# Kernel tuning notes

Hardware: AMD Instinct MI355X
Metric: run time of the kernel (lower is better)

The kernel has to match this reference:

```python
import jax, jax.numpy as jnp
import numpy as np

N = 50000      # nodes
E = 400000     # edges (avg degree 8)
N_IN = 256     # n_in_chan
N_HID = 256    # n_hid_chan


def gcn_conv(x, src, dst, W, b, n):
    """PyG GCNConv: D^{-1/2}(A+I)D^{-1/2} X W^T + b (add_self_loops=True, unit weights)."""
    h = x @ W.T                                           # [n, out]
    # degree over A + I: each node has a self loop (the initial ones) plus in-edges
    deg = jnp.ones((n,), h.dtype).at[dst].add(1.0)        # [n]
    dinv = jax.lax.rsqrt(deg)                             # deg >= 1 always
    norm = dinv[src] * dinv[dst]                          # [E]
    agg = jnp.zeros_like(h).at[dst].add(h[src] * norm[:, None])
    agg = agg + h * (dinv * dinv)[:, None]                # self-loop term, norm = dinv_i^2
    return agg + b


def setup_inputs() -> dict:
    key = jax.random.key(0)
    k1, k2, k3, k4 = jax.random.split(key, 4)
    x = jax.random.normal(k1, (N, N_IN + N_HID), dtype=jnp.float32)
    edge_index = jax.random.randint(k2, (2, E), 0, N, dtype=jnp.int64)
    s1 = 1.0 / np.sqrt(N_IN + N_HID)
    s2 = 1.0 / np.sqrt(N_HID)
    W1 = jax.random.normal(k3, (N_HID, N_IN + N_HID), dtype=jnp.float32) * s1
    W2 = jax.random.normal(k4, (N_HID, N_HID), dtype=jnp.float32) * s2
    b1 = jnp.zeros((N_HID,), jnp.float32)
    b2 = jnp.zeros((N_HID,), jnp.float32)
    return {"x": x, "edge_index": edge_index, "W1": W1, "b1": b1, "W2": W2, "b2": b2}


def reference(x, edge_index, W1, b1, W2, b2):
    src, dst = edge_index[0], edge_index[1]
    h = jax.nn.relu(gcn_conv(x, src, dst, W1, b1, N))
    return gcn_conv(h, src, dst, W2, b2, N)
```

## Files before the change

kernel.cpp:

```cpp
#include <hip/hip_runtime.h>

#define NN 50000
#define CH 256

typedef unsigned short u16;
typedef unsigned int   u32;

using short8 = __attribute__((ext_vector_type(8))) short;
using f32x4  = __attribute__((ext_vector_type(4))) float;

static __device__ __forceinline__ float4 ld4(const float* p){ return *(const float4*)p; }

static __device__ __forceinline__ u16 f2b(float f){
  u32 u = __float_as_uint(f);
  u = (u + 0x7fffu + ((u >> 16) & 1u)) >> 16;
  return (u16)u;
}
static __device__ __forceinline__ float b2f(u16 b){
  return __uint_as_float(((u32)b) << 16);
}


__global__ void hist_kernel(const int* __restrict__ dst, int* __restrict__ cnt, int E){
  int e = blockIdx.x*256 + threadIdx.x;
  if (e < E) atomicAdd(&cnt[dst[e]], 1);
}

__global__ void dinv_kernel(const int* __restrict__ cnt, float* __restrict__ dinv, int n){
  int i = blockIdx.x*256 + threadIdx.x;
  if (i < n) dinv[i] = rsqrtf(1.0f + (float)cnt[i]);
}

__global__ void scan_partial_kernel(const int* __restrict__ cnt, int* __restrict__ bsum, int n){
  __shared__ int sd[256];
  int t = threadIdx.x;
  int base = blockIdx.x*1024 + t*4;
  int s = 0;
  #pragma unroll
  for (int j=0;j<4;j++){ int idx = base+j; if (idx<n) s += cnt[idx]; }
  sd[t] = s; __syncthreads();
  for (int off=128; off>0; off>>=1){ if (t<off) sd[t]+=sd[t+off]; __syncthreads(); }
  if (t==0) bsum[blockIdx.x] = sd[0];
}

__global__ void scan_bsums_kernel(int* __restrict__ bsum, int nb){
  int t = threadIdx.x;
  int v = (t < nb) ? bsum[t] : 0;
  int orig = v;
  #pragma unroll
  for (int off=1; off<64; off<<=1){
    int u = __shfl_up(v, off, 64);
    if (t >= off) v += u;
  }
  if (t < nb) bsum[t] = v - orig;
}

__global__ void scan_final_kernel(const int* __restrict__ cnt, const int* __restrict__ bsum,
                                  int* __restrict__ offs, int* __restrict__ cursor, int n, int total){
  __shared__ int sd[256];
  int t = threadIdx.x;
  int base = blockIdx.x*1024 + t*4;
  int v[4]; int s=0;
  #pragma unroll
  for (int j=0;j<4;j++){ int idx=base+j; v[j] = (idx<n)?cnt[idx]:0; s += v[j]; }
  sd[t]=s; __syncthreads();
  for (int off=1; off<256; off<<=1){
    int x = (t>=off)? sd[t-off] : 0;
    __syncthreads();
    sd[t] += x;
    __syncthreads();
  }
  int run = bsum[blockIdx.x] + sd[t] - s;
  #pragma unroll
  for (int j=0;j<4;j++){
    int idx=base+j;
    if (idx<n){ offs[idx]=run; cursor[idx]=run; }
    run += v[j];
  }
  if (blockIdx.x==0 && t==0) offs[n] = total;
}

__global__ void scatter_kernel(const int* __restrict__ src, const int* __restrict__ dst,
                               const float* __restrict__ dinv, int* __restrict__ cursor,
                               int* __restrict__ esrc, float* __restrict__ enorm, int E){
  int e = blockIdx.x*256 + threadIdx.x;
  if (e < E){
    int d = dst[e], s = src[e];
    int pos = atomicAdd(&cursor[d], 1);
    esrc[pos] = s;
    enorm[pos] = dinv[s]*dinv[d];
  }
}


__global__ __launch_bounds__(256) void cvt_kernel(const float* __restrict__ in,
                                                  u16* __restrict__ out, int n4){
  int i = blockIdx.x*256 + threadIdx.x;
  if (i >= n4) return;
  float4 v = ld4(in + (size_t)i*4);
  ushort4 o;
  o.x = f2b(v.x); o.y = f2b(v.y); o.z = f2b(v.z); o.w = f2b(v.w);
  *(ushort4*)(out + (size_t)i*4) = o;
}


static __device__ __forceinline__ void gload_lds16(const u16* g, u16* l){
  __builtin_amdgcn_global_load_lds((const __attribute__((address_space(1))) void*)g,
                                   (__attribute__((address_space(3))) void*)l, 16, 0, 0);
}

__global__ __launch_bounds__(256) void gemm_mfma_kernel(const u16* __restrict__ A,
                                                        const u16* __restrict__ B,
                                                        u16* __restrict__ C,
                                                        int M, int K){
  __shared__ u16 As[128*32];
  __shared__ u16 Bs[128*32];
  int tid = threadIdx.x;
  int wave = tid >> 6, lane = tid & 63;
  int bm = blockIdx.x, bn = blockIdx.y;

  int sr = tid >> 2;
  int sc = (tid & 3) * 8;
  int ar0 = bm*128 + sr;       if (ar0 > M-1) ar0 = M-1;
  int ar1 = bm*128 + 64 + sr;  if (ar1 > M-1) ar1 = M-1;
  const u16* ga0 = A + (size_t)ar0*K + sc;
  const u16* ga1 = A + (size_t)ar1*K + sc;
  const u16* gb0 = B + (size_t)(bn*128 + sr)*K + sc;
  const u16* gb1 = B + (size_t)(bn*128 + 64 + sr)*K + sc;
  u16* la0 = As + (size_t)(wave*64)*8;
  u16* la1 = As + (size_t)(256 + wave*64)*8;
  u16* lb0 = Bs + (size_t)(wave*64)*8;
  u16* lb1 = Bs + (size_t)(256 + wave*64)*8;

  int wm = wave & 1, wn = wave >> 1;
  int lm = lane & 15;
  int lk = (lane >> 4) * 8;

  f32x4 acc[4][4] = {};

  for (int k0 = 0; k0 < K; k0 += 32){
    gload_lds16(ga0 + k0, la0);
    gload_lds16(ga1 + k0, la1);
    gload_lds16(gb0 + k0, lb0);
    gload_lds16(gb1 + k0, lb1);
    __syncthreads();
    short8 af[4], bfr[4];
    #pragma unroll
    for (int i=0;i<4;i++)
      af[i] = *(const short8*)&As[(size_t)(wm*64 + i*16 + lm)*32 + lk];
    #pragma unroll
    for (int j=0;j<4;j++)
      bfr[j] = *(const short8*)&Bs[(size_t)(wn*64 + j*16 + lm)*32 + lk];
    #pragma unroll
    for (int i=0;i<4;i++)
      #pragma unroll
      for (int j=0;j<4;j++)
        acc[i][j] = __builtin_amdgcn_mfma_f32_16x16x32_bf16(af[i], bfr[j], acc[i][j], 0, 0, 0);
    __syncthreads();
  }

  int rb = (lane >> 4) * 4;
  #pragma unroll
  for (int i=0;i<4;i++){
    #pragma unroll
    for (int r=0;r<4;r++){
      int row = bm*128 + wm*64 + i*16 + rb + r;
      if (row < M){
        #pragma unroll
        for (int j=0;j<4;j++){
          int col = bn*128 + wn*64 + j*16 + lm;
          C[(size_t)row*CH + col] = f2b(acc[i][j][r]);
        }
      }
    }
  }
}


template<bool RELU, bool OUTBF>
__global__ __launch_bounds__(256) void aggregate_kernel(const u16* __restrict__ h,
                                                        const float* __restrict__ bias,
                                                        const float* __restrict__ dinv,
                                                        const int* __restrict__ offs,
                                                        const int* __restrict__ esrc,
                                                        const float* __restrict__ enorm,
                                                        void* __restrict__ outv, int n){
  int wave = threadIdx.x >> 6;
  int lane = threadIdx.x & 63;
  int i = blockIdx.x*4 + wave;
  if (i >= n) return;
  int c = lane*4;
  float di = dinv[i];
  float w = di*di;
  float4 b4 = ld4(bias + c);
  ushort4 hv = *(const ushort4*)(h + (size_t)i*CH + c);
  float a0 = b2f(hv.x)*w + b4.x;
  float a1 = b2f(hv.y)*w + b4.y;
  float a2 = b2f(hv.z)*w + b4.z;
  float a3 = b2f(hv.w)*w + b4.w;
  int e0 = offs[i], e1 = offs[i+1];
  int e = e0;
  for (; e + 1 < e1; e += 2){
    int s0 = esrc[e], s1 = esrc[e+1];
    float n0 = enorm[e], n1 = enorm[e+1];
    ushort4 h0 = *(const ushort4*)(h + (size_t)s0*CH + c);
    ushort4 h1 = *(const ushort4*)(h + (size_t)s1*CH + c);
    a0 += b2f(h0.x)*n0; a1 += b2f(h0.y)*n0; a2 += b2f(h0.z)*n0; a3 += b2f(h0.w)*n0;
    a0 += b2f(h1.x)*n1; a1 += b2f(h1.y)*n1; a2 += b2f(h1.z)*n1; a3 += b2f(h1.w)*n1;
  }
  if (e < e1){
    int s0 = esrc[e];
    float n0 = enorm[e];
    ushort4 h0 = *(const ushort4*)(h + (size_t)s0*CH + c);
    a0 += b2f(h0.x)*n0; a1 += b2f(h0.y)*n0; a2 += b2f(h0.z)*n0; a3 += b2f(h0.w)*n0;
  }
  if (RELU){
    a0 = fmaxf(a0,0.f); a1 = fmaxf(a1,0.f); a2 = fmaxf(a2,0.f); a3 = fmaxf(a3,0.f);
  }
  if (OUTBF){
    ushort4 o; o.x=f2b(a0); o.y=f2b(a1); o.z=f2b(a2); o.w=f2b(a3);
    *(ushort4*)((u16*)outv + (size_t)i*CH + c) = o;
  } else {
    *(float4*)((float*)outv + (size_t)i*CH + c) = make_float4(a0,a1,a2,a3);
  }
}


extern "C" void kernel_launch(void* const* d_in, const int* in_sizes, int n_in,
                              void* d_out, int out_size, void* d_ws, size_t ws_size,
                              hipStream_t stream){
  const float* x  = (const float*)d_in[0];
  const int*   ei = (const int*)d_in[1];
  const float* W1 = (const float*)d_in[2];
  const float* b1 = (const float*)d_in[3];
  const float* W2 = (const float*)d_in[4];
  const float* b2 = (const float*)d_in[5];
  float* out = (float*)d_out;

  const int n = NN;
  const int E = in_sizes[1] / 2;
  const int* src = ei;
  const int* dst = ei + E;
  const int KIN = in_sizes[0] / n;

  char* ws = (char*)d_ws;
  size_t off = 0;
  auto alloc = [&](size_t bytes)->char* {
    char* p = ws + off;
    off += (bytes + 255) & ~(size_t)255;
    return p;
  };
  u16*   Xbf    = (u16*)  alloc((size_t)n*KIN*sizeof(u16));
  u16*   W1bf   = (u16*)  alloc((size_t)CH*KIN*sizeof(u16));
  u16*   W2bf   = (u16*)  alloc((size_t)CH*CH*sizeof(u16));
  float* dinv   = (float*)alloc((size_t)n*sizeof(float));
  int*   cnt    = (int*)  alloc((size_t)n*sizeof(int));
  int*   offs   = (int*)  alloc((size_t)(n+1)*sizeof(int));
  int*   cursor = (int*)  alloc((size_t)n*sizeof(int));
  int*   bsum   = (int*)  alloc(256*sizeof(int));
  int*   esrc   = (int*)  alloc((size_t)E*sizeof(int));
  float* enorm  = (float*)alloc((size_t)E*sizeof(float));
  (void)ws_size;

  u16* g1out = (u16*)d_out;
  u16* h1bf  = Xbf;
  u16* g2out = Xbf + (size_t)n*CH;

  hipMemsetAsync(cnt, 0, (size_t)n*sizeof(int), stream);
  hist_kernel<<<(E+255)/256, 256, 0, stream>>>(dst, cnt, E);
  dinv_kernel<<<(n+255)/256, 256, 0, stream>>>(cnt, dinv, n);
  int nb = (n + 1023) / 1024;
  scan_partial_kernel<<<nb, 256, 0, stream>>>(cnt, bsum, n);
  scan_bsums_kernel<<<1, 64, 0, stream>>>(bsum, nb);
  scan_final_kernel<<<nb, 256, 0, stream>>>(cnt, bsum, offs, cursor, n, E);
  scatter_kernel<<<(E+255)/256, 256, 0, stream>>>(src, dst, dinv, cursor, esrc, enorm, E);

  cvt_kernel<<<(n*KIN/4+255)/256, 256, 0, stream>>>(x, Xbf, n*KIN/4);
  cvt_kernel<<<(CH*KIN/4+255)/256, 256, 0, stream>>>(W1, W1bf, CH*KIN/4);
  cvt_kernel<<<(CH*CH/4+255)/256, 256, 0, stream>>>(W2, W2bf, CH*CH/4);

  dim3 gg((n+127)/128, CH/128);
  gemm_mfma_kernel<<<gg, 256, 0, stream>>>(Xbf, W1bf, g1out, n, KIN);
  aggregate_kernel<true, true><<<(n+3)/4, 256, 0, stream>>>(g1out, b1, dinv, offs, esrc, enorm, h1bf, n);

  gemm_mfma_kernel<<<gg, 256, 0, stream>>>(h1bf, W2bf, g2out, n, CH);
  aggregate_kernel<false, false><<<(n+3)/4, 256, 0, stream>>>(g2out, b2, dinv, offs, esrc, enorm, out, n);
}
```

Before: 356.9 us.

## Fuse graph setup and conversions into one cooperative kernel; widen aggregation loads

Replaces the histogram, dinv, three scan kernels, the CSR scatter and the three bf16 conversion kernels with a single cooperative-launch kernel that uses grid-wide syncs between phases. The X conversion overlaps with the block-sum scan. The aggregation kernel now gives each half-wave alternate edges, uses 8-wide bf16 loads and combines the halves with a cross-lane shuffle. The goal is to cut launch overhead and raise memory-level parallelism in the gather, at the cost of grid-sync latency and a fixed 512-block setup grid.

```diff
diff --git a/kernel.cpp b/kernel.cpp
--- a/kernel.cpp
+++ b/kernel.cpp
@@ -1,12 +1,17 @@
 #include <hip/hip_runtime.h>
+#include <hip/hip_cooperative_groups.h>
+
+namespace cg = cooperative_groups;
 
 #define NN 50000
 #define CH 256
+#define SETUP_BLOCKS 512
 
 typedef unsigned short u16;
 typedef unsigned int   u32;
 
 using short8 = __attribute__((ext_vector_type(8))) short;
+using u16x8  = __attribute__((ext_vector_type(8))) unsigned short;
 using f32x4  = __attribute__((ext_vector_type(4))) float;
 
 static __device__ __forceinline__ float4 ld4(const float* p){ return *(const float4*)p; }
@@ -21,86 +26,104 @@
 }
 
 
-__global__ void hist_kernel(const int* __restrict__ dst, int* __restrict__ cnt, int E){
-  int e = blockIdx.x*256 + threadIdx.x;
-  if (e < E) atomicAdd(&cnt[dst[e]], 1);
-}
-
-__global__ void dinv_kernel(const int* __restrict__ cnt, float* __restrict__ dinv, int n){
-  int i = blockIdx.x*256 + threadIdx.x;
-  if (i < n) dinv[i] = rsqrtf(1.0f + (float)cnt[i]);
-}
-
-__global__ void scan_partial_kernel(const int* __restrict__ cnt, int* __restrict__ bsum, int n){
+__global__ __launch_bounds__(256) void setup_kernel(const float* __restrict__ x,
+                                                    const float* __restrict__ W1,
+                                                    const float* __restrict__ W2,
+                                                    const int* __restrict__ src,
+                                                    const int* __restrict__ dst,
+                                                    u16* __restrict__ Xbf,
+                                                    u16* __restrict__ W1bf,
+                                                    u16* __restrict__ W2bf,
+                                                    float* __restrict__ dinv,
+                                                    int* __restrict__ cnt,
+                                                    int* __restrict__ offs,
+                                                    int* __restrict__ cursor,
+                                                    int* __restrict__ bsum,
+                                                    int* __restrict__ esrc,
+                                                    float* __restrict__ enorm,
+                                                    int n, int E, int KIN){
+  cg::grid_group grid = cg::this_grid();
   __shared__ int sd[256];
-  int t = threadIdx.x;
-  int base = blockIdx.x*1024 + t*4;
-  int s = 0;
-  #pragma unroll
-  for (int j=0;j<4;j++){ int idx = base+j; if (idx<n) s += cnt[idx]; }
-  sd[t] = s; __syncthreads();
-  for (int off=128; off>0; off>>=1){ if (t<off) sd[t]+=sd[t+off]; __syncthreads(); }
-  if (t==0) bsum[blockIdx.x] = sd[0];
-}
-
-__global__ void scan_bsums_kernel(int* __restrict__ bsum, int nb){
-  int t = threadIdx.x;
-  int v = (t < nb) ? bsum[t] : 0;
-  int orig = v;
-  #pragma unroll
-  for (int off=1; off<64; off<<=1){
-    int u = __shfl_up(v, off, 64);
-    if (t >= off) v += u;
-  }
-  if (t < nb) bsum[t] = v - orig;
-}
-
-__global__ void scan_final_kernel(const int* __restrict__ cnt, const int* __restrict__ bsum,
-                                  int* __restrict__ offs, int* __restrict__ cursor, int n, int total){
-  __shared__ int sd[256];
-  int t = threadIdx.x;
-  int base = blockIdx.x*1024 + t*4;
-  int v[4]; int s=0;
-  #pragma unroll
-  for (int j=0;j<4;j++){ int idx=base+j; v[j] = (idx<n)?cnt[idx]:0; s += v[j]; }
-  sd[t]=s; __syncthreads();
-  for (int off=1; off<256; off<<=1){
-    int x = (t>=off)? sd[t-off] : 0;
-    __syncthreads();
-    sd[t] += x;
-    __syncthreads();
-  }
-  int run = bsum[blockIdx.x] + sd[t] - s;
-  #pragma unroll
-  for (int j=0;j<4;j++){
-    int idx=base+j;
-    if (idx<n){ offs[idx]=run; cursor[idx]=run; }
-    run += v[j];
-  }
-  if (blockIdx.x==0 && t==0) offs[n] = total;
-}
-
-__global__ void scatter_kernel(const int* __restrict__ src, const int* __restrict__ dst,
-                               const float* __restrict__ dinv, int* __restrict__ cursor,
-                               int* __restrict__ esrc, float* __restrict__ enorm, int E){
-  int e = blockIdx.x*256 + threadIdx.x;
-  if (e < E){
+  const int t = threadIdx.x;
+  const int b = blockIdx.x;
+  const int T = gridDim.x * 256;
+  const int g = b*256 + t;
+  const int nb2 = (n + 255) / 256;
+
+  for (int i = g; i < n; i += T) cnt[i] = 0;
+  int w1n = CH*KIN/4;
+  for (int i = g; i < w1n; i += T){
+    float4 v = ld4(W1 + (size_t)i*4);
+    ushort4 o; o.x=f2b(v.x); o.y=f2b(v.y); o.z=f2b(v.z); o.w=f2b(v.w);
+    *(ushort4*)(W1bf + (size_t)i*4) = o;
+  }
+  int w2n = CH*CH/4;
+  for (int i = g; i < w2n; i += T){
+    float4 v = ld4(W2 + (size_t)i*4);
+    ushort4 o; o.x=f2b(v.x); o.y=f2b(v.y); o.z=f2b(v.z); o.w=f2b(v.w);
+    *(ushort4*)(W2bf + (size_t)i*4) = o;
+  }
+  grid.sync();
+
+  for (int e = g; e < E; e += T) atomicAdd(&cnt[dst[e]], 1);
+  grid.sync();
+
+  if (b < nb2){
+    int i = b*256 + t;
+    int v = (i < n) ? cnt[i] : 0;
+    if (i < n) dinv[i] = rsqrtf(1.0f + (float)v);
+    sd[t] = v; __syncthreads();
+    #pragma unroll
+    for (int off=1; off<256; off<<=1){
+      int u = (t>=off) ? sd[t-off] : 0;
+      __syncthreads();
+      sd[t] += u;
+      __syncthreads();
+    }
+    if (i < n) offs[i] = sd[t];
+    if (t == 255) bsum[b] = sd[255];
+  }
+  grid.sync();
+
+  if (b == 0){
+    int v = (t < nb2) ? bsum[t] : 0;
+    sd[t] = v; __syncthreads();
+    #pragma unroll
+    for (int off=1; off<256; off<<=1){
+      int u = (t>=off) ? sd[t-off] : 0;
+      __syncthreads();
+      sd[t] += u;
+      __syncthreads();
+    }
+    if (t < nb2) bsum[t] = sd[t] - v;
+  } else {
+    int xn = n*(KIN/4);
+    int T3 = (gridDim.x-1)*256;
+    for (int i = (b-1)*256 + t; i < xn; i += T3){
+      float4 v = ld4(x + (size_t)i*4);
+      ushort4 o; o.x=f2b(v.x); o.y=f2b(v.y); o.z=f2b(v.z); o.w=f2b(v.w);
+      *(ushort4*)(Xbf + (size_t)i*4) = o;
+    }
+  }
+  grid.sync();
+
+  if (b < nb2){
+    int i = b*256 + t;
+    if (i < n){
+      int ex = bsum[b] + offs[i] - cnt[i];
+      offs[i] = ex;
+      cursor[i] = ex;
+    }
+  }
+  if (g == 0) offs[n] = E;
+  grid.sync();
+
+  for (int e = g; e < E; e += T){
     int d = dst[e], s = src[e];
     int pos = atomicAdd(&cursor[d], 1);
     esrc[pos] = s;
     enorm[pos] = dinv[s]*dinv[d];
   }
-}
-
-
-__global__ __launch_bounds__(256) void cvt_kernel(const float* __restrict__ in,
-                                                  u16* __restrict__ out, int n4){
-  int i = blockIdx.x*256 + threadIdx.x;
-  if (i >= n4) return;
-  float4 v = ld4(in + (size_t)i*4);
-  ushort4 o;
-  o.x = f2b(v.x); o.y = f2b(v.y); o.z = f2b(v.z); o.w = f2b(v.w);
-  *(ushort4*)(out + (size_t)i*4) = o;
 }
 
 
@@ -189,39 +212,62 @@
   int lane = threadIdx.x & 63;
   int i = blockIdx.x*4 + wave;
   if (i >= n) return;
-  int c = lane*4;
-  float di = dinv[i];
-  float w = di*di;
-  float4 b4 = ld4(bias + c);
-  ushort4 hv = *(const ushort4*)(h + (size_t)i*CH + c);
-  float a0 = b2f(hv.x)*w + b4.x;
-  float a1 = b2f(hv.y)*w + b4.y;
-  float a2 = b2f(hv.z)*w + b4.z;
-  float a3 = b2f(hv.w)*w + b4.w;
+  int half = lane >> 5;
+  int c = (lane & 31) * 8;
+
+  float acc[8];
+  u16x8 hv = *(const u16x8*)(h + (size_t)i*CH + c);
+  if (half == 0){
+    float di = dinv[i];
+    float w = di*di;
+    float4 b0 = ld4(bias + c), b1 = ld4(bias + c + 4);
+    acc[0]=b2f(hv[0])*w+b0.x; acc[1]=b2f(hv[1])*w+b0.y;
+    acc[2]=b2f(hv[2])*w+b0.z; acc[3]=b2f(hv[3])*w+b0.w;
+    acc[4]=b2f(hv[4])*w+b1.x; acc[5]=b2f(hv[5])*w+b1.y;
+    acc[6]=b2f(hv[6])*w+b1.z; acc[7]=b2f(hv[7])*w+b1.w;
+  } else {
+    #pragma unroll
+    for (int k=0;k<8;k++) acc[k] = 0.f;
+  }
+
   int e0 = offs[i], e1 = offs[i+1];
-  int e = e0;
-  for (; e + 1 < e1; e += 2){
-    int s0 = esrc[e], s1 = esrc[e+1];
-    float n0 = enorm[e], n1 = enorm[e+1];
-    ushort4 h0 = *(const ushort4*)(h + (size_t)s0*CH + c);
-    ushort4 h1 = *(const ushort4*)(h + (size_t)s1*CH + c);
-    a0 += b2f(h0.x)*n0; a1 += b2f(h0.y)*n0; a2 += b2f(h0.z)*n0; a3 += b2f(h0.w)*n0;
-    a0 += b2f(h1.x)*n1; a1 += b2f(h1.y)*n1; a2 += b2f(h1.z)*n1; a3 += b2f(h1.w)*n1;
+  int e = e0 + half;
+  for (; e + 2 < e1; e += 4){
+    int sA = esrc[e],   sB = esrc[e+2];
+    float nA = enorm[e], nB = enorm[e+2];
+    u16x8 hA = *(const u16x8*)(h + (size_t)sA*CH + c);
+    u16x8 hB = *(const u16x8*)(h + (size_t)sB*CH + c);
+    #pragma unroll
+    for (int k=0;k<8;k++) acc[k] += b2f(hA[k])*nA;
+    #pragma unroll
+    for (int k=0;k<8;k++) acc[k] += b2f(hB[k])*nB;
   }
   if (e < e1){
-    int s0 = esrc[e];
-    float n0 = enorm[e];
-    ushort4 h0 = *(const ushort4*)(h + (size_t)s0*CH + c);
-    a0 += b2f(h0.x)*n0; a1 += b2f(h0.y)*n0; a2 += b2f(h0.z)*n0; a3 += b2f(h0.w)*n0;
-  }
-  if (RELU){
-    a0 = fmaxf(a0,0.f); a1 = fmaxf(a1,0.f); a2 = fmaxf(a2,0.f); a3 = fmaxf(a3,0.f);
-  }
-  if (OUTBF){
-    ushort4 o; o.x=f2b(a0); o.y=f2b(a1); o.z=f2b(a2); o.w=f2b(a3);
-    *(ushort4*)((u16*)outv + (size_t)i*CH + c) = o;
-  } else {
-    *(float4*)((float*)outv + (size_t)i*CH + c) = make_float4(a0,a1,a2,a3);
+    int sA = esrc[e];
+    float nA = enorm[e];
+    u16x8 hA = *(const u16x8*)(h + (size_t)sA*CH + c);
+    #pragma unroll
+    for (int k=0;k<8;k++) acc[k] += b2f(hA[k])*nA;
+  }
+
+  #pragma unroll
+  for (int k=0;k<8;k++) acc[k] += __shfl_xor(acc[k], 32, 64);
+
+  if (half == 0){
+    if (RELU){
+      #pragma unroll
+      for (int k=0;k<8;k++) acc[k] = fmaxf(acc[k], 0.f);
+    }
+    if (OUTBF){
+      u16x8 o;
+      #pragma unroll
+      for (int k=0;k<8;k++) o[k] = f2b(acc[k]);
+      *(u16x8*)((u16*)outv + (size_t)i*CH + c) = o;
+    } else {
+      float* op = (float*)outv + (size_t)i*CH + c;
+      *(float4*)op       = make_float4(acc[0],acc[1],acc[2],acc[3]);
+      *(float4*)(op + 4) = make_float4(acc[4],acc[5],acc[6],acc[7]);
+    }
   }
 }
 
@@ -266,18 +312,16 @@
   u16* h1bf  = Xbf;
   u16* g2out = Xbf + (size_t)n*CH;
 
-  hipMemsetAsync(cnt, 0, (size_t)n*sizeof(int), stream);
-  hist_kernel<<<(E+255)/256, 256, 0, stream>>>(dst, cnt, E);
-  dinv_kernel<<<(n+255)/256, 256, 0, stream>>>(cnt, dinv, n);
-  int nb = (n + 1023) / 1024;
-  scan_partial_kernel<<<nb, 256, 0, stream>>>(cnt, bsum, n);
-  scan_bsums_kernel<<<1, 64, 0, stream>>>(bsum, nb);
-  scan_final_kernel<<<nb, 256, 0, stream>>>(cnt, bsum, offs, cursor, n, E);
-  scatter_kernel<<<(E+255)/256, 256, 0, stream>>>(src, dst, dinv, cursor, esrc, enorm, E);
-
-  cvt_kernel<<<(n*KIN/4+255)/256, 256, 0, stream>>>(x, Xbf, n*KIN/4);
-  cvt_kernel<<<(CH*KIN/4+255)/256, 256, 0, stream>>>(W1, W1bf, CH*KIN/4);
-  cvt_kernel<<<(CH*CH/4+255)/256, 256, 0, stream>>>(W2, W2bf, CH*CH/4);
+  {
+    int nn = n, EE = E, KK = KIN;
+    void* args[] = { (void*)&x, (void*)&W1, (void*)&W2, (void*)&src, (void*)&dst,
+                     (void*)&Xbf, (void*)&W1bf, (void*)&W2bf,
+                     (void*)&dinv, (void*)&cnt, (void*)&offs, (void*)&cursor,
+                     (void*)&bsum, (void*)&esrc, (void*)&enorm,
+                     (void*)&nn, (void*)&EE, (void*)&KK };
+    hipLaunchCooperativeKernel((const void*)setup_kernel, dim3(SETUP_BLOCKS), dim3(256),
+                               args, 0, stream);
+  }
 
   dim3 gg((n+127)/128, CH/128);
   gemm_mfma_kernel<<<gg, 256, 0, stream>>>(Xbf, W1bf, g1out, n, KIN);
```

Measured after the change: 631.6 us. 77.0% more time.

## Split edges across half-waves with 16-byte gathers, fuse dinv and conversion kernels

Applied to the files above, without the earlier changes.

The aggregate kernel now gives each half-wave alternate edges, so each lane loads 8 bf16 channels (16 bytes) per gather with four gathers in flight. The two halves are combined with a cross-lane shuffle before the output is written. The dinv computation is folded into the scan partial kernel, and the three fp32-to-bf16 conversions are merged into one grid-stride launch of 512 blocks, removing several small launches. The trade-offs are that half the lanes sit idle during the epilogue, and the fixed 512-block grid-stride conversion may use bandwidth less well than the previous one-element-per-thread grid.

```diff
diff --git a/kernel.cpp b/kernel.cpp
--- a/kernel.cpp
+++ b/kernel.cpp
@@ -7,6 +7,7 @@
 typedef unsigned int   u32;
 
 using short8 = __attribute__((ext_vector_type(8))) short;
+using u16x8  = __attribute__((ext_vector_type(8))) unsigned short;
 using f32x4  = __attribute__((ext_vector_type(4))) float;
 
 static __device__ __forceinline__ float4 ld4(const float* p){ return *(const float4*)p; }
@@ -26,18 +27,21 @@
   if (e < E) atomicAdd(&cnt[dst[e]], 1);
 }
 
-__global__ void dinv_kernel(const int* __restrict__ cnt, float* __restrict__ dinv, int n){
-  int i = blockIdx.x*256 + threadIdx.x;
-  if (i < n) dinv[i] = rsqrtf(1.0f + (float)cnt[i]);
-}
-
-__global__ void scan_partial_kernel(const int* __restrict__ cnt, int* __restrict__ bsum, int n){
+__global__ void scan_partial_kernel(const int* __restrict__ cnt, int* __restrict__ bsum,
+                                    float* __restrict__ dinv, int n){
   __shared__ int sd[256];
   int t = threadIdx.x;
   int base = blockIdx.x*1024 + t*4;
   int s = 0;
   #pragma unroll
-  for (int j=0;j<4;j++){ int idx = base+j; if (idx<n) s += cnt[idx]; }
+  for (int j=0;j<4;j++){
+    int idx = base+j;
+    if (idx<n){
+      int v = cnt[idx];
+      s += v;
+      dinv[idx] = rsqrtf(1.0f + (float)v);
+    }
+  }
   sd[t] = s; __syncthreads();
   for (int off=128; off>0; off>>=1){ if (t<off) sd[t]+=sd[t+off]; __syncthreads(); }
   if (t==0) bsum[blockIdx.x] = sd[0];
@@ -93,14 +97,26 @@
 }
 
 
-__global__ __launch_bounds__(256) void cvt_kernel(const float* __restrict__ in,
-                                                  u16* __restrict__ out, int n4){
-  int i = blockIdx.x*256 + threadIdx.x;
-  if (i >= n4) return;
-  float4 v = ld4(in + (size_t)i*4);
-  ushort4 o;
-  o.x = f2b(v.x); o.y = f2b(v.y); o.z = f2b(v.z); o.w = f2b(v.w);
-  *(ushort4*)(out + (size_t)i*4) = o;
+__global__ __launch_bounds__(256) void cvt_all_kernel(const float* __restrict__ x,  u16* __restrict__ Xbf,  int xn4,
+                                                      const float* __restrict__ w1, u16* __restrict__ W1bf, int w1n4,
+                                                      const float* __restrict__ w2, u16* __restrict__ W2bf, int w2n4){
+  int T = gridDim.x * 256;
+  int g = blockIdx.x*256 + threadIdx.x;
+  for (int i = g; i < xn4; i += T){
+    float4 v = ld4(x + (size_t)i*4);
+    ushort4 o; o.x=f2b(v.x); o.y=f2b(v.y); o.z=f2b(v.z); o.w=f2b(v.w);
+    *(ushort4*)(Xbf + (size_t)i*4) = o;
+  }
+  for (int i = g; i < w1n4; i += T){
+    float4 v = ld4(w1 + (size_t)i*4);
+    ushort4 o; o.x=f2b(v.x); o.y=f2b(v.y); o.z=f2b(v.z); o.w=f2b(v.w);
+    *(ushort4*)(W1bf + (size_t)i*4) = o;
+  }
+  for (int i = g; i < w2n4; i += T){
+    float4 v = ld4(w2 + (size_t)i*4);
+    ushort4 o; o.x=f2b(v.x); o.y=f2b(v.y); o.z=f2b(v.z); o.w=f2b(v.w);
+    *(ushort4*)(W2bf + (size_t)i*4) = o;
+  }
 }
 
 
@@ -189,39 +205,68 @@
   int lane = threadIdx.x & 63;
   int i = blockIdx.x*4 + wave;
   if (i >= n) return;
-  int c = lane*4;
-  float di = dinv[i];
-  float w = di*di;
-  float4 b4 = ld4(bias + c);
-  ushort4 hv = *(const ushort4*)(h + (size_t)i*CH + c);
-  float a0 = b2f(hv.x)*w + b4.x;
-  float a1 = b2f(hv.y)*w + b4.y;
-  float a2 = b2f(hv.z)*w + b4.z;
-  float a3 = b2f(hv.w)*w + b4.w;
+  int half = lane >> 5;
+  int c = (lane & 31) * 8;
+
+  float acc[8];
+  #pragma unroll
+  for (int k=0;k<8;k++) acc[k] = 0.f;
+
   int e0 = offs[i], e1 = offs[i+1];
-  int e = e0;
-  for (; e + 1 < e1; e += 2){
-    int s0 = esrc[e], s1 = esrc[e+1];
-    float n0 = enorm[e], n1 = enorm[e+1];
-    ushort4 h0 = *(const ushort4*)(h + (size_t)s0*CH + c);
-    ushort4 h1 = *(const ushort4*)(h + (size_t)s1*CH + c);
-    a0 += b2f(h0.x)*n0; a1 += b2f(h0.y)*n0; a2 += b2f(h0.z)*n0; a3 += b2f(h0.w)*n0;
-    a0 += b2f(h1.x)*n1; a1 += b2f(h1.y)*n1; a2 += b2f(h1.z)*n1; a3 += b2f(h1.w)*n1;
-  }
-  if (e < e1){
+  int e = e0 + half;
+  for (; e + 6 < e1; e += 8){
+    int s0 = esrc[e],   s1 = esrc[e+2], s2 = esrc[e+4], s3 = esrc[e+6];
+    float n0 = enorm[e], n1 = enorm[e+2], n2 = enorm[e+4], n3 = enorm[e+6];
+    u16x8 h0 = *(const u16x8*)(h + (size_t)s0*CH + c);
+    u16x8 h1 = *(const u16x8*)(h + (size_t)s1*CH + c);
+    u16x8 h2 = *(const u16x8*)(h + (size_t)s2*CH + c);
+    u16x8 h3 = *(const u16x8*)(h + (size_t)s3*CH + c);
+    #pragma unroll
+    for (int k=0;k<8;k++) acc[k] += b2f(h0[k])*n0;
+    #pragma unroll
+    for (int k=0;k<8;k++) acc[k] += b2f(h1[k])*n1;
+    #pragma unroll
+    for (int k=0;k<8;k++) acc[k] += b2f(h2[k])*n2;
+    #pragma unroll
+    for (int k=0;k<8;k++) acc[k] += b2f(h3[k])*n3;
+  }
+  for (; e < e1; e += 2){
     int s0 = esrc[e];
     float n0 = enorm[e];
-    ushort4 h0 = *(const ushort4*)(h + (size_t)s0*CH + c);
-    a0 += b2f(h0.x)*n0; a1 += b2f(h0.y)*n0; a2 += b2f(h0.z)*n0; a3 += b2f(h0.w)*n0;
-  }
-  if (RELU){
-    a0 = fmaxf(a0,0.f); a1 = fmaxf(a1,0.f); a2 = fmaxf(a2,0.f); a3 = fmaxf(a3,0.f);
-  }
-  if (OUTBF){
-    ushort4 o; o.x=f2b(a0); o.y=f2b(a1); o.z=f2b(a2); o.w=f2b(a3);
-    *(ushort4*)((u16*)outv + (size_t)i*CH + c) = o;
-  } else {
-    *(float4*)((float*)outv + (size_t)i*CH + c) = make_float4(a0,a1,a2,a3);
+    u16x8 h0 = *(const u16x8*)(h + (size_t)s0*CH + c);
+    #pragma unroll
+    for (int k=0;k<8;k++) acc[k] += b2f(h0[k])*n0;
+  }
+
+  if (half == 0){
+    float di = dinv[i];
+    float w = di*di;
+    float4 b0 = ld4(bias + c), b1 = ld4(bias + c + 4);
+    u16x8 hv = *(const u16x8*)(h + (size_t)i*CH + c);
+    acc[0] += b2f(hv[0])*w + b0.x; acc[1] += b2f(hv[1])*w + b0.y;
+    acc[2] += b2f(hv[2])*w + b0.z; acc[3] += b2f(hv[3])*w + b0.w;
+    acc[4] += b2f(hv[4])*w + b1.x; acc[5] += b2f(hv[5])*w + b1.y;
+    acc[6] += b2f(hv[6])*w + b1.z; acc[7] += b2f(hv[7])*w + b1.w;
+  }
+
+  #pragma unroll
+  for (int k=0;k<8;k++) acc[k] += __shfl_xor(acc[k], 32, 64);
+
+  if (half == 0){
+    if (RELU){
+      #pragma unroll
+      for (int k=0;k<8;k++) acc[k] = fmaxf(acc[k], 0.f);
+    }
+    if (OUTBF){
+      u16x8 o;
+      #pragma unroll
+      for (int k=0;k<8;k++) o[k] = f2b(acc[k]);
+      *(u16x8*)((u16*)outv + (size_t)i*CH + c) = o;
+    } else {
+      float* op = (float*)outv + (size_t)i*CH + c;
+      *(float4*)op       = make_float4(acc[0],acc[1],acc[2],acc[3]);
+      *(float4*)(op + 4) = make_float4(acc[4],acc[5],acc[6],acc[7]);
+    }
   }
 }
 
@@ -268,16 +313,13 @@
 
   hipMemsetAsync(cnt, 0, (size_t)n*sizeof(int), stream);
   hist_kernel<<<(E+255)/256, 256, 0, stream>>>(dst, cnt, E);
-  dinv_kernel<<<(n+255)/256, 256, 0, stream>>>(cnt, dinv, n);
   int nb = (n + 1023) / 1024;
-  scan_partial_kernel<<<nb, 256, 0, stream>>>(cnt, bsum, n);
+  scan_partial_kernel<<<nb, 256, 0, stream>>>(cnt, bsum, dinv, n);
   scan_bsums_kernel<<<1, 64, 0, stream>>>(bsum, nb);
   scan_final_kernel<<<nb, 256, 0, stream>>>(cnt, bsum, offs, cursor, n, E);
   scatter_kernel<<<(E+255)/256, 256, 0, stream>>>(src, dst, dinv, cursor, esrc, enorm, E);
 
-  cvt_kernel<<<(n*KIN/4+255)/256, 256, 0, stream>>>(x, Xbf, n*KIN/4);
-  cvt_kernel<<<(CH*KIN/4+255)/256, 256, 0, stream>>>(W1, W1bf, CH*KIN/4);
-  cvt_kernel<<<(CH*CH/4+255)/256, 256, 0, stream>>>(W2, W2bf, CH*CH/4);
+  cvt_all_kernel<<<512, 256, 0, stream>>>(x, Xbf, n*KIN/4, W1, W1bf, CH*KIN/4, W2, W2bf, CH*CH/4);
 
   dim3 gg((n+127)/128, CH/128);
   gemm_mfma_kernel<<<gg, 256, 0, stream>>>(Xbf, W1bf, g1out, n, KIN);
```

Result: no change. 355.2 us (-0.5%).
